# Kernel tuning notes

Hardware: AMD Instinct MI355X
Metric: run time of the kernel (lower is better)

## Reference

```python
import jax, jax.numpy as jnp
import numpy as np
from jax import lax


def setup_inputs() -> dict:
    key = jax.random.key(0)
    k1, k2 = jax.random.split(key)
    B, C, H, W = 4, 128, 128, 256
    features_1 = jax.random.normal(k1, (B, C, H, W), dtype=jnp.float32)
    features_2 = jax.random.normal(k2, (B, C, H, W), dtype=jnp.float32)
    return {"features_1": features_1, "features_2": features_2, "lvls": 64}


def reference(features_1, features_2, lvls):
    # Cost volume: cost[b, i, h, w] = mean_c f1[b,c,h,w] * f2[b,c,h,w-i] for w >= i, else 0.
    B, C, H, W = features_1.shape
    # Left-pad f2 along width with (lvls-1) zeros so shifted slices are static-size.
    f2_pad = jnp.pad(features_2, ((0, 0), (0, 0), (0, 0), (lvls - 1, 0)))

    def body(carry, i):
        # slice starting at (lvls-1-i) gives f2 shifted right by disparity i, zeros where w < i
        f2_shift = lax.dynamic_slice_in_dim(f2_pad, lvls - 1 - i, W, axis=3)
        cost_i = jnp.mean(features_1 * f2_shift, axis=1)  # [B, H, W]
        return carry, cost_i

    _, cost = lax.scan(body, None, jnp.arange(lvls))  # [lvls, B, H, W]
    return jnp.moveaxis(cost, 0, 1)  # [B, lvls, H, W]
```

## Files before the change

### kernel.cpp

```cpp
#include <hip/hip_runtime.h>
#include <hip/hip_bf16.h>


#define BDIM 4
#define CDIM 128
#define HDIM 128
#define WDIM 256
#define LVLS 64
#define HW   (HDIM * WDIM)
#define CHW  (CDIM * HDIM * WDIM)
#define NWORK (BDIM * HDIM * 8)
#define NBLK  (NWORK / 2)

typedef short    bf16x8 __attribute__((ext_vector_type(8)));
typedef float    f32x16 __attribute__((ext_vector_type(16)));
typedef float    f32x4  __attribute__((ext_vector_type(4)));

__device__ __forceinline__ short f2bf(float f) {
    __hip_bfloat16 h = __float2bfloat16(f);
    return __builtin_bit_cast(short, h);
}

__device__ __forceinline__ void lds_fence() {
    asm volatile("s_waitcnt lgkmcnt(0)" ::: "memory");
    __builtin_amdgcn_sched_barrier(0);
}

__global__ __launch_bounds__(128, 8) void cost_volume_kernel(
    const float* __restrict__ f1, const float* __restrict__ f2,
    float* __restrict__ out)
{
    __shared__ float strips[2][LVLS * 32];

    const int tid  = threadIdx.x;
    const int lane = tid & 63;
    const int wv   = tid >> 6;

    const int bid  = blockIdx.x;
    const int work = ((bid & 7) * (NBLK / 8) + (bid >> 3)) * 2 + wv;

    const int wt = work & 7;
    const int h  = (work >> 3) & (HDIM - 1);
    const int b  = work >> 10;

    float* strip = strips[wv];

    const float* __restrict__ f1bh = f1 + (size_t)b * CHW + (size_t)h * WDIM;
    const float* __restrict__ f2bh = f2 + (size_t)b * CHW + (size_t)h * WDIM;

    const int wl    = lane & 31;
    const int wglob = wt * 32 + wl;
    const int koff  = (lane >> 5) * 8;

    const int c0 = ((wt - 2 < 0) ? 0 : wt - 2) * 32 + wl;
    const int c1 = ((wt - 1 < 0) ? 0 : wt - 1) * 32 + wl;
    const int c2 = wt * 32 + wl;

    f32x16 acc0 = (f32x16)0.0f, acc1 = (f32x16)0.0f, acc2 = (f32x16)0.0f;

    const float* pB  = f1bh + (size_t)koff * HW + wglob;
    const float* pA0 = f2bh + (size_t)koff * HW + c0;
    const float* pA1 = f2bh + (size_t)koff * HW + c1;
    const float* pA2 = f2bh + (size_t)koff * HW + c2;

    #pragma unroll
    for (int kk = 0; kk < 8; ++kk) {
        const size_t kb = (size_t)(kk * 16) * HW;

        float rb[8], ra0[8], ra1[8], ra2[8];
        #pragma unroll
        for (int j = 0; j < 8; ++j) rb[j]  = pB [kb + (size_t)j * HW];
        #pragma unroll
        for (int j = 0; j < 8; ++j) ra0[j] = pA0[kb + (size_t)j * HW];
        #pragma unroll
        for (int j = 0; j < 8; ++j) ra1[j] = pA1[kb + (size_t)j * HW];
        #pragma unroll
        for (int j = 0; j < 8; ++j) ra2[j] = pA2[kb + (size_t)j * HW];

        bf16x8 fb, fa0, fa1, fa2;
        #pragma unroll
        for (int j = 0; j < 8; ++j) {
            fb[j]  = f2bf(rb[j]);
            fa0[j] = f2bf(ra0[j]);
            fa1[j] = f2bf(ra1[j]);
            fa2[j] = f2bf(ra2[j]);
        }

        acc0 = __builtin_amdgcn_mfma_f32_32x32x16_bf16(fa0, fb, acc0, 0, 0, 0);
        acc1 = __builtin_amdgcn_mfma_f32_32x32x16_bf16(fa1, fb, acc1, 0, 0, 0);
        acc2 = __builtin_amdgcn_mfma_f32_32x32x16_bf16(fa2, fb, acc2, 0, 0, 0);
    }


    #pragma unroll
    for (int it = 0; it < 8; ++it)
        reinterpret_cast<f32x4*>(strip)[it * 64 + lane] = (f32x4)0.0f;

    lds_fence();

    const int rbase = 4 * (lane >> 5);
    {
        const f32x16* accs[3] = { &acc0, &acc1, &acc2 };
        #pragma unroll
        for (int t = 0; t < 3; ++t) {
            const int tp = wt - 2 + t;
            if (tp >= 0) {
                const f32x16 a = *accs[t];
                #pragma unroll
                for (int r = 0; r < 16; ++r) {
                    const int prow = tp * 32 + (r & 3) + 8 * (r >> 2) + rbase;
                    const int i = wglob - prow;
                    if (i >= 0 && i < LVLS)
                        strip[i * 32 + wl] = a[r] * (1.0f / CDIM);
                }
            }
        }
    }

    lds_fence();

    const size_t obase = (size_t)b * LVLS * HW + (size_t)h * WDIM + wt * 32;
    #pragma unroll
    for (int it = 0; it < 8; ++it) {
        const int idx = it * 64 + lane;
        const int row = idx >> 3;
        const int w4  = idx & 7;
        const f32x4 v = *reinterpret_cast<const f32x4*>(&strip[row * 32 + w4 * 4]);
        __builtin_nontemporal_store(v, reinterpret_cast<f32x4*>(out + obase + (size_t)row * HW + w4 * 4));
    }
}

extern "C" void kernel_launch(void* const* d_in, const int* in_sizes, int n_in,
                              void* d_out, int out_size, void* d_ws, size_t ws_size,
                              hipStream_t stream) {
    const float* f1 = (const float*)d_in[0];
    const float* f2 = (const float*)d_in[1];
    float* out = (float*)d_out;
    cost_volume_kernel<<<dim3(NBLK), dim3(128), 0, stream>>>(f1, f2, out);
}
```

Measured before the change: 30.02 us.

## Split each output tile's three MFMA chains across two waves sharing an LDS strip

Each block now handles one (b,h,wt) tile with two waves instead of two independent tiles with one wave each. Wave 0 computes the diagonal and previous-tile products, and wave 1 computes the tile two columns back. Both scatter into one shared LDS strip and each writes half the output rows, using __syncthreads in place of per-wave lgkmcnt waits. This shortens the per-wave dependency chain and doubles the block count, at the cost of loading the f1 tile twice, adding block barriers, and leaving wave 1 idle for tiles wt<2.

```diff
diff --git a/kernel.cpp b/kernel.cpp
--- a/kernel.cpp
+++ b/kernel.cpp
@@ -10,7 +10,6 @@
 #define HW   (HDIM * WDIM)
 #define CHW  (CDIM * HDIM * WDIM)
 #define NWORK (BDIM * HDIM * 8)
-#define NBLK  (NWORK / 2)
 
 typedef short    bf16x8 __attribute__((ext_vector_type(8)));
 typedef float    f32x16 __attribute__((ext_vector_type(16)));
@@ -21,29 +20,22 @@
     return __builtin_bit_cast(short, h);
 }
 
-__device__ __forceinline__ void lds_fence() {
-    asm volatile("s_waitcnt lgkmcnt(0)" ::: "memory");
-    __builtin_amdgcn_sched_barrier(0);
-}
-
 __global__ __launch_bounds__(128, 8) void cost_volume_kernel(
     const float* __restrict__ f1, const float* __restrict__ f2,
     float* __restrict__ out)
 {
-    __shared__ float strips[2][LVLS * 32];
+    __shared__ float strip[LVLS * 32];
 
     const int tid  = threadIdx.x;
     const int lane = tid & 63;
     const int wv   = tid >> 6;
 
     const int bid  = blockIdx.x;
-    const int work = ((bid & 7) * (NBLK / 8) + (bid >> 3)) * 2 + wv;
+    const int unit = (bid & 7) * (NWORK / 8) + (bid >> 3);
 
-    const int wt = work & 7;
-    const int h  = (work >> 3) & (HDIM - 1);
-    const int b  = work >> 10;
-
-    float* strip = strips[wv];
+    const int wt = unit & 7;
+    const int h  = (unit >> 3) & (HDIM - 1);
+    const int b  = unit >> 10;
 
     const float* __restrict__ f1bh = f1 + (size_t)b * CHW + (size_t)h * WDIM;
     const float* __restrict__ f2bh = f2 + (size_t)b * CHW + (size_t)h * WDIM;
@@ -52,77 +44,96 @@
     const int wglob = wt * 32 + wl;
     const int koff  = (lane >> 5) * 8;
 
-    const int c0 = ((wt - 2 < 0) ? 0 : wt - 2) * 32 + wl;
-    const int c1 = ((wt - 1 < 0) ? 0 : wt - 1) * 32 + wl;
-    const int c2 = wt * 32 + wl;
+    f32x16 accA = (f32x16)0.0f, accB = (f32x16)0.0f;
 
-    f32x16 acc0 = (f32x16)0.0f, acc1 = (f32x16)0.0f, acc2 = (f32x16)0.0f;
+    if (wv == 0) {
+        const int ca = ((wt - 1 < 0) ? 0 : wt - 1) * 32 + wl;
+        const int cb = wt * 32 + wl;
+        const float* pB  = f1bh + (size_t)koff * HW + wglob;
+        const float* pAa = f2bh + (size_t)koff * HW + ca;
+        const float* pAb = f2bh + (size_t)koff * HW + cb;
 
-    const float* pB  = f1bh + (size_t)koff * HW + wglob;
-    const float* pA0 = f2bh + (size_t)koff * HW + c0;
-    const float* pA1 = f2bh + (size_t)koff * HW + c1;
-    const float* pA2 = f2bh + (size_t)koff * HW + c2;
+        #pragma unroll
+        for (int kk = 0; kk < 8; ++kk) {
+            const size_t kb = (size_t)(kk * 16) * HW;
+            float rb[8], raa[8], rab[8];
+            #pragma unroll
+            for (int j = 0; j < 8; ++j) rb[j]  = pB [kb + (size_t)j * HW];
+            #pragma unroll
+            for (int j = 0; j < 8; ++j) raa[j] = pAa[kb + (size_t)j * HW];
+            #pragma unroll
+            for (int j = 0; j < 8; ++j) rab[j] = pAb[kb + (size_t)j * HW];
 
-    #pragma unroll
-    for (int kk = 0; kk < 8; ++kk) {
-        const size_t kb = (size_t)(kk * 16) * HW;
+            bf16x8 fb, faa, fab;
+            #pragma unroll
+            for (int j = 0; j < 8; ++j) {
+                fb[j]  = f2bf(rb[j]);
+                faa[j] = f2bf(raa[j]);
+                fab[j] = f2bf(rab[j]);
+            }
+            accA = __builtin_amdgcn_mfma_f32_32x32x16_bf16(faa, fb, accA, 0, 0, 0);
+            accB = __builtin_amdgcn_mfma_f32_32x32x16_bf16(fab, fb, accB, 0, 0, 0);
+        }
+    } else if (wt >= 2) {
+        const int ca = (wt - 2) * 32 + wl;
+        const float* pB  = f1bh + (size_t)koff * HW + wglob;
+        const float* pAa = f2bh + (size_t)koff * HW + ca;
 
-        float rb[8], ra0[8], ra1[8], ra2[8];
         #pragma unroll
-        for (int j = 0; j < 8; ++j) rb[j]  = pB [kb + (size_t)j * HW];
-        #pragma unroll
-        for (int j = 0; j < 8; ++j) ra0[j] = pA0[kb + (size_t)j * HW];
-        #pragma unroll
-        for (int j = 0; j < 8; ++j) ra1[j] = pA1[kb + (size_t)j * HW];
-        #pragma unroll
-        for (int j = 0; j < 8; ++j) ra2[j] = pA2[kb + (size_t)j * HW];
+        for (int kk = 0; kk < 8; ++kk) {
+            const size_t kb = (size_t)(kk * 16) * HW;
+            float rb[8], raa[8];
+            #pragma unroll
+            for (int j = 0; j < 8; ++j) rb[j]  = pB [kb + (size_t)j * HW];
+            #pragma unroll
+            for (int j = 0; j < 8; ++j) raa[j] = pAa[kb + (size_t)j * HW];
 
-        bf16x8 fb, fa0, fa1, fa2;
-        #pragma unroll
-        for (int j = 0; j < 8; ++j) {
-            fb[j]  = f2bf(rb[j]);
-            fa0[j] = f2bf(ra0[j]);
-            fa1[j] = f2bf(ra1[j]);
-            fa2[j] = f2bf(ra2[j]);
+            bf16x8 fb, faa;
+            #pragma unroll
+            for (int j = 0; j < 8; ++j) {
+                fb[j]  = f2bf(rb[j]);
+                faa[j] = f2bf(raa[j]);
+            }
+            accA = __builtin_amdgcn_mfma_f32_32x32x16_bf16(faa, fb, accA, 0, 0, 0);
         }
-
-        acc0 = __builtin_amdgcn_mfma_f32_32x32x16_bf16(fa0, fb, acc0, 0, 0, 0);
-        acc1 = __builtin_amdgcn_mfma_f32_32x32x16_bf16(fa1, fb, acc1, 0, 0, 0);
-        acc2 = __builtin_amdgcn_mfma_f32_32x32x16_bf16(fa2, fb, acc2, 0, 0, 0);
     }
 
 
     #pragma unroll
-    for (int it = 0; it < 8; ++it)
-        reinterpret_cast<f32x4*>(strip)[it * 64 + lane] = (f32x4)0.0f;
+    for (int it = 0; it < 4; ++it)
+        reinterpret_cast<f32x4*>(strip)[(wv * 4 + it) * 64 + lane] = (f32x4)0.0f;
 
-    lds_fence();
+    __syncthreads();
 
     const int rbase = 4 * (lane >> 5);
     {
-        const f32x16* accs[3] = { &acc0, &acc1, &acc2 };
-        #pragma unroll
-        for (int t = 0; t < 3; ++t) {
-            const int tp = wt - 2 + t;
-            if (tp >= 0) {
-                const f32x16 a = *accs[t];
-                #pragma unroll
-                for (int r = 0; r < 16; ++r) {
-                    const int prow = tp * 32 + (r & 3) + 8 * (r >> 2) + rbase;
-                    const int i = wglob - prow;
-                    if (i >= 0 && i < LVLS)
-                        strip[i * 32 + wl] = a[r] * (1.0f / CDIM);
-                }
+        const int tpA = (wv == 0) ? wt - 1 : wt - 2;
+        if (tpA >= 0) {
+            #pragma unroll
+            for (int r = 0; r < 16; ++r) {
+                const int prow = tpA * 32 + (r & 3) + 8 * (r >> 2) + rbase;
+                const int i = wglob - prow;
+                if (i >= 0 && i < LVLS)
+                    strip[i * 32 + wl] = accA[r] * (1.0f / CDIM);
+            }
+        }
+        if (wv == 0) {
+            #pragma unroll
+            for (int r = 0; r < 16; ++r) {
+                const int prow = wt * 32 + (r & 3) + 8 * (r >> 2) + rbase;
+                const int i = wglob - prow;
+                if (i >= 0 && i < LVLS)
+                    strip[i * 32 + wl] = accB[r] * (1.0f / CDIM);
             }
         }
     }
 
-    lds_fence();
+    __syncthreads();
 
     const size_t obase = (size_t)b * LVLS * HW + (size_t)h * WDIM + wt * 32;
     #pragma unroll
-    for (int it = 0; it < 8; ++it) {
-        const int idx = it * 64 + lane;
+    for (int it = 0; it < 4; ++it) {
+        const int idx = (wv * 4 + it) * 64 + lane;
         const int row = idx >> 3;
         const int w4  = idx & 7;
         const f32x4 v = *reinterpret_cast<const f32x4*>(&strip[row * 32 + w4 * 4]);
@@ -136,5 +147,5 @@
     const float* f1 = (const float*)d_in[0];
     const float* f2 = (const float*)d_in[1];
     float* out = (float*)d_out;
-    cost_volume_kernel<<<dim3(NBLK), dim3(128), 0, stream>>>(f1, f2, out);
+    cost_volume_kernel<<<dim3(NWORK), dim3(128), 0, stream>>>(f1, f2, out);
 }
```

After: 39.85 us. 1.33x slower.
